# Kernel optimization log

Hardware: AMD Instinct MI355X
Metric: run time of the kernel (lower is better)

## Reference

```python
import jax, jax.numpy as jnp
import numpy as np
import math

H = 1024
N2 = 32  # N // 2 complex modes
L_LEN = 4096
LOG_DT_MIN = math.log(0.001)
LOG_DT_MAX = math.log(0.1)


def setup_inputs() -> dict:
    key = jax.random.key(0)
    k1, k2 = jax.random.split(key, 2)
    # log_dt ~ Uniform(log dt_min, log dt_max)
    log_dt = jax.random.uniform(k1, (H,), dtype=jnp.float32) * (LOG_DT_MAX - LOG_DT_MIN) + LOG_DT_MIN
    # C stored as real view of complex (H, N2): last dim = (real, imag)
    C = jax.random.normal(k2, (H, N2, 2), dtype=jnp.float32)
    log_A_real = jnp.log(0.5 * jnp.ones((H, N2), dtype=jnp.float32))
    A_imag = (math.pi * jnp.arange(N2, dtype=jnp.float32))[None, :] * jnp.ones((H, 1), jnp.float32)
    return {"log_dt": log_dt, "C": C, "log_A_real": log_A_real, "A_imag": A_imag, "L": L_LEN}


def reference(log_dt, C, log_A_real, A_imag, L):
    # dt: (H,)
    dt = jnp.exp(log_dt)
    # complex C: (H, N2)
    Cc = C[..., 0] + 1j * C[..., 1]
    # A = -exp(log_A_real) + i*A_imag : (H, N2)
    A = -jnp.exp(log_A_real) + 1j * A_imag
    dtA = A * dt[:, None]  # (H, N2)
    # discretized coefficient: C * (exp(dtA)-1)/A  (ZOH-like)
    Ck = Cc * (jnp.exp(dtA) - 1.0) / A  # (H, N2)
    # Vandermonde: exp(dtA * l) for l in [0, L)  -> (H, N2, L)
    V = jnp.exp(dtA[..., None] * jnp.arange(L, dtype=jnp.float32))
    # K = 2 * Re( sum_n Ck[h,n] * V[h,n,l] )  -> (H, L)
    K = 2.0 * jnp.einsum('hn,hnl->hl', Ck, V).real
    return K
```

## Files before the change

kernel.cpp:

```cpp
#include <hip/hip_runtime.h>
#include <math.h>


#define N2 32
#define L_LEN 4096
#define NTHREADS 256
#define JTILE (L_LEN / NTHREADS)

__global__ __launch_bounds__(NTHREADS) void s4d_gen_kernel(
    const float* __restrict__ log_dt,
    const float* __restrict__ Cri,
    const float* __restrict__ log_A_real,
    const float* __restrict__ A_imag,
    float* __restrict__ out)
{
  const int h = blockIdx.x;
  const int t = threadIdx.x;

  __shared__ double s_yrev[N2];
  __shared__ float s_x[N2], s_ckr[N2], s_cki[N2];
  __shared__ float s_Wr[N2], s_Wi[N2], s_p[N2], s_q[N2];

  if (t < N2) {
    const int n = t;
    const double dt = exp((double)log_dt[h]);
    const double Ar = -exp((double)log_A_real[h * N2 + n]);
    const double Ai = (double)A_imag[h * N2 + n];
    const double xr = dt * Ar;
    const double xi = dt * Ai;
    const double ex = exp(xr);
    const double wr = ex * cos(xi);
    const double wi = ex * sin(xi);
    const double nr = wr - 1.0, ni = wi;
    const double inv = 1.0 / (Ar * Ar + Ai * Ai);
    const double fr = (nr * Ar + ni * Ai) * inv;
    const double fi = (ni * Ar - nr * Ai) * inv;
    const double c0 = (double)Cri[(h * N2 + n) * 2 + 0];
    const double c1 = (double)Cri[(h * N2 + n) * 2 + 1];
    s_ckr[n] = (float)(2.0 * (c0 * fr - c1 * fi));
    s_cki[n] = (float)(2.0 * (c0 * fi + c1 * fr));
    s_x[n]    = (float)xr;
    s_yrev[n] = xi * 0.15915494309189535;
    double ar = wr, ai2 = wi;
#pragma unroll
    for (int k = 0; k < 8; ++k) {
      const double tr = ar * ar - ai2 * ai2;
      const double ti = 2.0 * ar * ai2;
      ar = tr; ai2 = ti;
    }
    s_Wr[n] = (float)ar;
    s_Wi[n] = (float)ai2;
    s_p[n]  = (float)(2.0 * ar);
    s_q[n]  = (float)(ar * ar + ai2 * ai2);
  }
  __syncthreads();

  float acc[JTILE];
#pragma unroll
  for (int j = 0; j < JTILE; ++j) acc[j] = 0.0f;

  const float  tf = (float)t;
  const double td = (double)t;

  for (int n = 0; n < N2; ++n) {
    double ph = s_yrev[n] * td;
    ph -= floor(ph);
    const float frac = (float)ph;
    const float sn = __builtin_amdgcn_sinf(frac);
    const float cs = __builtin_amdgcn_cosf(frac);
    const float e  = __expf(s_x[n] * tf);
    const float vr = e * cs;
    const float vi = e * sn;
    const float ckr = s_ckr[n], cki = s_cki[n];
    const float ur = fmaf(ckr, vr, -(cki * vi));
    const float ui = fmaf(ckr, vi,  cki * vr);
    float s0 = ur;
    float s1 = fmaf(ur, s_Wr[n], -(ui * s_Wi[n]));
    acc[0] += s0;
    acc[1] += s1;
    const float p = s_p[n], q = s_q[n];
#pragma unroll
    for (int j = 2; j < JTILE; ++j) {
      const float s2 = fmaf(p, s1, -(q * s0));
      acc[j] += s2;
      s0 = s1; s1 = s2;
    }
  }

  float* o = out + (size_t)h * L_LEN + t;
#pragma unroll
  for (int j = 0; j < JTILE; ++j) o[j * NTHREADS] = acc[j];
}

extern "C" void kernel_launch(void* const* d_in, const int* in_sizes, int n_in,
                              void* d_out, int out_size, void* d_ws, size_t ws_size,
                              hipStream_t stream) {
  const float* log_dt     = (const float*)d_in[0];
  const float* Cri        = (const float*)d_in[1];
  const float* log_A_real = (const float*)d_in[2];
  const float* A_imag     = (const float*)d_in[3];
  float* out = (float*)d_out;
  const int H = in_sizes[0];

  s4d_gen_kernel<<<dim3(H), dim3(NTHREADS), 0, stream>>>(
      log_dt, Cri, log_A_real, A_imag, out);
}
```

Before: 79.50 us.

## Split coefficient prep into separate kernel and split sequence length across blocks

Per-mode FP64 coefficient setup moves out of each block into a separate fully parallel prep kernel. Previously only 32 of 256 threads did this work while the rest waited at a barrier. Results go to workspace in global memory as a packed struct plus a double array. The main kernel now uses a 2D grid, with each block covering half of the sequence and each thread computing 8 outputs instead of 16. This doubles the blocks for occupancy, but also doubles the per-mode transcendental setup per output and adds a second launch and global coefficient reads.

```diff
diff --git a/kernel.cpp b/kernel.cpp
--- a/kernel.cpp
+++ b/kernel.cpp
@@ -5,89 +5,103 @@
 #define N2 32
 #define L_LEN 4096
 #define NTHREADS 256
-#define JTILE (L_LEN / NTHREADS)
+#define JTILE 8
+#define HALF_L 2048
 
-__global__ __launch_bounds__(NTHREADS) void s4d_gen_kernel(
+struct Coef {
+  float x;
+  float ckr, cki;
+  float Wr, Wi;
+  float p, q;
+  float pad;
+};
+
+__global__ __launch_bounds__(256) void s4d_prep_kernel(
     const float* __restrict__ log_dt,
     const float* __restrict__ Cri,
     const float* __restrict__ log_A_real,
     const float* __restrict__ A_imag,
+    double* __restrict__ yrev,
+    Coef* __restrict__ cf)
+{
+  const int idx = blockIdx.x * 256 + threadIdx.x;
+  const int h = idx >> 5;
+
+  const double dt = exp((double)log_dt[h]);
+  const double Ar = -exp((double)log_A_real[idx]);
+  const double Ai = (double)A_imag[idx];
+  const double xr = dt * Ar;
+  const double xi = dt * Ai;
+  const double ex = exp(xr);
+  const double wr = ex * cos(xi);
+  const double wi = ex * sin(xi);
+  const double nr = wr - 1.0, ni = wi;
+  const double inv = 1.0 / (Ar * Ar + Ai * Ai);
+  const double fr = (nr * Ar + ni * Ai) * inv;
+  const double fi = (ni * Ar - nr * Ai) * inv;
+  const double c0 = (double)Cri[idx * 2 + 0];
+  const double c1 = (double)Cri[idx * 2 + 1];
+  double ar = wr, ai = wi;
+#pragma unroll
+  for (int k = 0; k < 8; ++k) {
+    const double tr = ar * ar - ai * ai;
+    const double ti = 2.0 * ar * ai;
+    ar = tr; ai = ti;
+  }
+  Coef c;
+  c.x   = (float)xr;
+  c.ckr = (float)(2.0 * (c0 * fr - c1 * fi));
+  c.cki = (float)(2.0 * (c0 * fi + c1 * fr));
+  c.Wr  = (float)ar;
+  c.Wi  = (float)ai;
+  c.p   = (float)(2.0 * ar);
+  c.q   = (float)(ar * ar + ai * ai);
+  c.pad = 0.0f;
+  cf[idx] = c;
+  yrev[idx] = xi * 0.15915494309189535;
+}
+
+__global__ __launch_bounds__(NTHREADS) void s4d_main_kernel(
+    const double* __restrict__ yrev,
+    const Coef* __restrict__ cf,
     float* __restrict__ out)
 {
   const int h = blockIdx.x;
-  const int t = threadIdx.x;
-
-  __shared__ double s_yrev[N2];
-  __shared__ float s_x[N2], s_ckr[N2], s_cki[N2];
-  __shared__ float s_Wr[N2], s_Wi[N2], s_p[N2], s_q[N2];
-
-  if (t < N2) {
-    const int n = t;
-    const double dt = exp((double)log_dt[h]);
-    const double Ar = -exp((double)log_A_real[h * N2 + n]);
-    const double Ai = (double)A_imag[h * N2 + n];
-    const double xr = dt * Ar;
-    const double xi = dt * Ai;
-    const double ex = exp(xr);
-    const double wr = ex * cos(xi);
-    const double wi = ex * sin(xi);
-    const double nr = wr - 1.0, ni = wi;
-    const double inv = 1.0 / (Ar * Ar + Ai * Ai);
-    const double fr = (nr * Ar + ni * Ai) * inv;
-    const double fi = (ni * Ar - nr * Ai) * inv;
-    const double c0 = (double)Cri[(h * N2 + n) * 2 + 0];
-    const double c1 = (double)Cri[(h * N2 + n) * 2 + 1];
-    s_ckr[n] = (float)(2.0 * (c0 * fr - c1 * fi));
-    s_cki[n] = (float)(2.0 * (c0 * fi + c1 * fr));
-    s_x[n]    = (float)xr;
-    s_yrev[n] = xi * 0.15915494309189535;
-    double ar = wr, ai2 = wi;
-#pragma unroll
-    for (int k = 0; k < 8; ++k) {
-      const double tr = ar * ar - ai2 * ai2;
-      const double ti = 2.0 * ar * ai2;
-      ar = tr; ai2 = ti;
-    }
-    s_Wr[n] = (float)ar;
-    s_Wi[n] = (float)ai2;
-    s_p[n]  = (float)(2.0 * ar);
-    s_q[n]  = (float)(ar * ar + ai2 * ai2);
-  }
-  __syncthreads();
+  const int l0 = blockIdx.y * HALF_L + threadIdx.x;
+  const float  lf = (float)l0;
+  const double ld = (double)l0;
 
   float acc[JTILE];
 #pragma unroll
   for (int j = 0; j < JTILE; ++j) acc[j] = 0.0f;
 
-  const float  tf = (float)t;
-  const double td = (double)t;
-
+  const int base = h * N2;
+#pragma unroll 4
   for (int n = 0; n < N2; ++n) {
-    double ph = s_yrev[n] * td;
+    const Coef c = cf[base + n];
+    double ph = yrev[base + n] * ld;
     ph -= floor(ph);
     const float frac = (float)ph;
     const float sn = __builtin_amdgcn_sinf(frac);
     const float cs = __builtin_amdgcn_cosf(frac);
-    const float e  = __expf(s_x[n] * tf);
+    const float e  = __expf(c.x * lf);
     const float vr = e * cs;
     const float vi = e * sn;
-    const float ckr = s_ckr[n], cki = s_cki[n];
-    const float ur = fmaf(ckr, vr, -(cki * vi));
-    const float ui = fmaf(ckr, vi,  cki * vr);
+    const float ur = fmaf(c.ckr, vr, -(c.cki * vi));
+    const float ui = fmaf(c.ckr, vi,  c.cki * vr);
     float s0 = ur;
-    float s1 = fmaf(ur, s_Wr[n], -(ui * s_Wi[n]));
+    float s1 = fmaf(ur, c.Wr, -(ui * c.Wi));
     acc[0] += s0;
     acc[1] += s1;
-    const float p = s_p[n], q = s_q[n];
 #pragma unroll
     for (int j = 2; j < JTILE; ++j) {
-      const float s2 = fmaf(p, s1, -(q * s0));
+      const float s2 = fmaf(c.p, s1, -(c.q * s0));
       acc[j] += s2;
       s0 = s1; s1 = s2;
     }
   }
 
-  float* o = out + (size_t)h * L_LEN + t;
+  float* o = out + (size_t)h * L_LEN + l0;
 #pragma unroll
   for (int j = 0; j < JTILE; ++j) o[j * NTHREADS] = acc[j];
 }
@@ -102,6 +116,10 @@
   float* out = (float*)d_out;
   const int H = in_sizes[0];
 
-  s4d_gen_kernel<<<dim3(H), dim3(NTHREADS), 0, stream>>>(
-      log_dt, Cri, log_A_real, A_imag, out);
+  double* yrev = (double*)d_ws;
+  Coef*   cf   = (Coef*)((char*)d_ws + (size_t)H * N2 * sizeof(double));
+
+  s4d_prep_kernel<<<dim3(H * N2 / 256), dim3(256), 0, stream>>>(
+      log_dt, Cri, log_A_real, A_imag, yrev, cf);
+  s4d_main_kernel<<<dim3(H, 2), dim3(NTHREADS), 0, stream>>>(yrev, cf, out);
 }
```

Result: slower. 86.41 us (+8.7%).

## Factor Vandermonde into power tables and evaluate via per-thread dot products

Applied to the files above, without the earlier changes.

Splits the work into a prep kernel and a main kernel. The prep kernel computes per-mode power tables W^(16a), Ck·W^b and W^(256j) into the workspace. The main kernel forms W^(16a+b) products per thread and reduces over modes with dot products against the W^256 table, replacing the per-thread sin/cos/exp and the second-order recurrence. This adds a second launch, workspace traffic, and float power accumulation whose error may grow for large exponents.

```diff
diff --git a/kernel.cpp b/kernel.cpp
--- a/kernel.cpp
+++ b/kernel.cpp
@@ -5,91 +5,128 @@
 #define N2 32
 #define L_LEN 4096
 #define NTHREADS 256
-#define JTILE (L_LEN / NTHREADS)
 
-__global__ __launch_bounds__(NTHREADS) void s4d_gen_kernel(
+#define PQ_STRIDE 32
+#define A2OFF (1024 * 1024)
+
+__global__ __launch_bounds__(256) void s4d_prep_kernel(
     const float* __restrict__ log_dt,
     const float* __restrict__ Cri,
     const float* __restrict__ log_A_real,
     const float* __restrict__ A_imag,
+    float2* __restrict__ ws2)
+{
+  const int idx = blockIdx.x * 256 + threadIdx.x;
+  const int h = idx >> 5;
+  const int n = idx & 31;
+
+  const double dt = exp((double)log_dt[h]);
+  const double Ar = -exp((double)log_A_real[idx]);
+  const double Ai = (double)A_imag[idx];
+  const double xr = dt * Ar;
+  const double xi = dt * Ai;
+  const double ex = exp(xr);
+  const double wr = ex * cos(xi);
+  const double wi = ex * sin(xi);
+  const double nr = wr - 1.0, ni = wi;
+  const double inv = 1.0 / (Ar * Ar + Ai * Ai);
+  const double fr = (nr * Ar + ni * Ai) * inv;
+  const double fi = (ni * Ar - nr * Ai) * inv;
+  const double c0 = (double)Cri[idx * 2 + 0];
+  const double c1 = (double)Cri[idx * 2 + 1];
+  const float ckr = (float)(2.0 * (c0 * fr - c1 * fi));
+  const float cki = (float)(2.0 * (c0 * fi + c1 * fr));
+
+  double ar = wr, ai2 = wi;
+#pragma unroll
+  for (int k = 0; k < 4; ++k) {
+    const double tr = ar * ar - ai2 * ai2;
+    const double ti = 2.0 * ar * ai2;
+    ar = tr; ai2 = ti;
+  }
+  const float w16r = (float)ar, w16i = (float)ai2;
+#pragma unroll
+  for (int k = 0; k < 4; ++k) {
+    const double tr = ar * ar - ai2 * ai2;
+    const double ti = 2.0 * ar * ai2;
+    ar = tr; ai2 = ti;
+  }
+  const float w256r = (float)ar, w256i = (float)ai2;
+  const float wfr = (float)wr, wfi = (float)wi;
+
+  float2* pq = ws2 + (size_t)idx * PQ_STRIDE;
+  float pr = 1.0f, pi = 0.0f;
+#pragma unroll
+  for (int a = 0; a < 16; ++a) {
+    pq[a] = make_float2(pr, pi);
+    const float tr = fmaf(pr, w16r, -(pi * w16i));
+    const float ti = fmaf(pr, w16i, pi * w16r);
+    pr = tr; pi = ti;
+  }
+  float qr = ckr, qi = cki;
+#pragma unroll
+  for (int b = 0; b < 16; ++b) {
+    pq[16 + b] = make_float2(qr, qi);
+    const float tr = fmaf(qr, wfr, -(qi * wfi));
+    const float ti = fmaf(qr, wfi, qi * wfr);
+    qr = tr; qi = ti;
+  }
+  float2* a2 = ws2 + A2OFF + (size_t)h * (16 * N2) + n;
+  float sr = 1.0f, si = 0.0f;
+#pragma unroll
+  for (int j = 0; j < 16; ++j) {
+    a2[j * N2] = make_float2(sr, si);
+    const float tr = fmaf(sr, w256r, -(si * w256i));
+    const float ti = fmaf(sr, w256i, si * w256r);
+    sr = tr; si = ti;
+  }
+}
+
+__global__ __launch_bounds__(NTHREADS, 4) void s4d_main_kernel(
+    const float2* __restrict__ ws2,
     float* __restrict__ out)
 {
   const int h = blockIdx.x;
   const int t = threadIdx.x;
+  const int a = t >> 4;
+  const int b = t & 15;
 
-  __shared__ double s_yrev[N2];
-  __shared__ float s_x[N2], s_ckr[N2], s_cki[N2];
-  __shared__ float s_Wr[N2], s_Wi[N2], s_p[N2], s_q[N2];
-
-  if (t < N2) {
-    const int n = t;
-    const double dt = exp((double)log_dt[h]);
-    const double Ar = -exp((double)log_A_real[h * N2 + n]);
-    const double Ai = (double)A_imag[h * N2 + n];
-    const double xr = dt * Ar;
-    const double xi = dt * Ai;
-    const double ex = exp(xr);
-    const double wr = ex * cos(xi);
-    const double wi = ex * sin(xi);
-    const double nr = wr - 1.0, ni = wi;
-    const double inv = 1.0 / (Ar * Ar + Ai * Ai);
-    const double fr = (nr * Ar + ni * Ai) * inv;
-    const double fi = (ni * Ar - nr * Ai) * inv;
-    const double c0 = (double)Cri[(h * N2 + n) * 2 + 0];
-    const double c1 = (double)Cri[(h * N2 + n) * 2 + 1];
-    s_ckr[n] = (float)(2.0 * (c0 * fr - c1 * fi));
-    s_cki[n] = (float)(2.0 * (c0 * fi + c1 * fr));
-    s_x[n]    = (float)xr;
-    s_yrev[n] = xi * 0.15915494309189535;
-    double ar = wr, ai2 = wi;
+  __shared__ float2 sPQ[N2 * PQ_STRIDE];
+  {
+    const float4* src = (const float4*)(ws2 + (size_t)h * N2 * PQ_STRIDE);
+    float4* dst = (float4*)sPQ;
 #pragma unroll
-    for (int k = 0; k < 8; ++k) {
-      const double tr = ar * ar - ai2 * ai2;
-      const double ti = 2.0 * ar * ai2;
-      ar = tr; ai2 = ti;
-    }
-    s_Wr[n] = (float)ar;
-    s_Wi[n] = (float)ai2;
-    s_p[n]  = (float)(2.0 * ar);
-    s_q[n]  = (float)(ar * ar + ai2 * ai2);
+    for (int i = 0; i < 2; ++i) dst[t + i * NTHREADS] = src[t + i * NTHREADS];
   }
   __syncthreads();
 
-  float acc[JTILE];
+  float br[N2], bi[N2];
 #pragma unroll
-  for (int j = 0; j < JTILE; ++j) acc[j] = 0.0f;
+  for (int n = 0; n < N2; ++n) {
+    const float2 P = sPQ[n * PQ_STRIDE + a];
+    const float2 Q = sPQ[n * PQ_STRIDE + 16 + b];
+    br[n] = fmaf(P.x, Q.x, -(P.y * Q.y));
+    bi[n] = fmaf(P.x, Q.y, P.y * Q.x);
+  }
 
-  const float  tf = (float)t;
-  const double td = (double)t;
-
-  for (int n = 0; n < N2; ++n) {
-    double ph = s_yrev[n] * td;
-    ph -= floor(ph);
-    const float frac = (float)ph;
-    const float sn = __builtin_amdgcn_sinf(frac);
-    const float cs = __builtin_amdgcn_cosf(frac);
-    const float e  = __expf(s_x[n] * tf);
-    const float vr = e * cs;
-    const float vi = e * sn;
-    const float ckr = s_ckr[n], cki = s_cki[n];
-    const float ur = fmaf(ckr, vr, -(cki * vi));
-    const float ui = fmaf(ckr, vi,  cki * vr);
-    float s0 = ur;
-    float s1 = fmaf(ur, s_Wr[n], -(ui * s_Wi[n]));
-    acc[0] += s0;
-    acc[1] += s1;
-    const float p = s_p[n], q = s_q[n];
+  const float2* a2h = ws2 + A2OFF + (size_t)h * (16 * N2);
+  float acc[16];
+#pragma unroll 4
+  for (int j = 0; j < 16; ++j) {
+    const float2* row = a2h + j * N2;
+    float s = 0.0f;
 #pragma unroll
-    for (int j = 2; j < JTILE; ++j) {
-      const float s2 = fmaf(p, s1, -(q * s0));
-      acc[j] += s2;
-      s0 = s1; s1 = s2;
+    for (int n = 0; n < N2; ++n) {
+      const float2 a2 = row[n];
+      s = fmaf(a2.x, br[n], s);
+      s = fmaf(-a2.y, bi[n], s);
     }
+    acc[j] = s;
   }
 
   float* o = out + (size_t)h * L_LEN + t;
 #pragma unroll
-  for (int j = 0; j < JTILE; ++j) o[j * NTHREADS] = acc[j];
+  for (int j = 0; j < 16; ++j) o[j * NTHREADS] = acc[j];
 }
 
 extern "C" void kernel_launch(void* const* d_in, const int* in_sizes, int n_in,
@@ -102,6 +139,9 @@
   float* out = (float*)d_out;
   const int H = in_sizes[0];
 
-  s4d_gen_kernel<<<dim3(H), dim3(NTHREADS), 0, stream>>>(
-      log_dt, Cri, log_A_real, A_imag, out);
+  float2* ws2 = (float2*)d_ws;
+
+  s4d_prep_kernel<<<dim3(H * N2 / 256), dim3(256), 0, stream>>>(
+      log_dt, Cri, log_A_real, A_imag, ws2);
+  s4d_main_kernel<<<dim3(H), dim3(NTHREADS), 0, stream>>>(ws2, out);
 }
```

After: 159.0 us. 2x slower.

## Replace per-thread transcendental phase with precomputed power tables in shared memory

Applied to the files above, without the earlier changes.

Each thread's starting value w^t was previously computed with a double-precision phase reduction plus sin, cos and exp for every mode. It is now formed as a product of two table entries, P[a]=w^(16a) and Q[b]=Ck*w^b, where t=16a+b. Two warps fill these tables in shared memory, so the main loop needs only a complex multiply per mode. This removes the double-precision floor and the transcendental calls from the hot loop, at the cost of an extra barrier and shared-memory traffic. Accuracy may differ because the powers are built by repeated float multiplication. The launch bounds also add a minimum-blocks hint.

```diff
diff --git a/kernel.cpp b/kernel.cpp
--- a/kernel.cpp
+++ b/kernel.cpp
@@ -5,9 +5,8 @@
 #define N2 32
 #define L_LEN 4096
 #define NTHREADS 256
-#define JTILE (L_LEN / NTHREADS)
 
-__global__ __launch_bounds__(NTHREADS) void s4d_gen_kernel(
+__global__ __launch_bounds__(NTHREADS, 4) void s4d_fused_kernel(
     const float* __restrict__ log_dt,
     const float* __restrict__ Cri,
     const float* __restrict__ log_A_real,
@@ -16,16 +15,20 @@
 {
   const int h = blockIdx.x;
   const int t = threadIdx.x;
+  const int a = t >> 4;
+  const int b = t & 15;
 
-  __shared__ double s_yrev[N2];
-  __shared__ float s_x[N2], s_ckr[N2], s_cki[N2];
-  __shared__ float s_Wr[N2], s_Wi[N2], s_p[N2], s_q[N2];
+  __shared__ float2 s_w[N2], s_w16[N2], s_ck[N2];
+  __shared__ float4 s_Wpq[N2];
+  __shared__ float2 s_P[16 * N2];
+  __shared__ float2 s_Q[16 * N2];
 
   if (t < N2) {
     const int n = t;
+    const int idx = h * N2 + n;
     const double dt = exp((double)log_dt[h]);
-    const double Ar = -exp((double)log_A_real[h * N2 + n]);
-    const double Ai = (double)A_imag[h * N2 + n];
+    const double Ar = -exp((double)log_A_real[idx]);
+    const double Ai = (double)A_imag[idx];
     const double xr = dt * Ar;
     const double xi = dt * Ai;
     const double ex = exp(xr);
@@ -35,53 +38,78 @@
     const double inv = 1.0 / (Ar * Ar + Ai * Ai);
     const double fr = (nr * Ar + ni * Ai) * inv;
     const double fi = (ni * Ar - nr * Ai) * inv;
-    const double c0 = (double)Cri[(h * N2 + n) * 2 + 0];
-    const double c1 = (double)Cri[(h * N2 + n) * 2 + 1];
-    s_ckr[n] = (float)(2.0 * (c0 * fr - c1 * fi));
-    s_cki[n] = (float)(2.0 * (c0 * fi + c1 * fr));
-    s_x[n]    = (float)xr;
-    s_yrev[n] = xi * 0.15915494309189535;
+    const double c0 = (double)Cri[idx * 2 + 0];
+    const double c1 = (double)Cri[idx * 2 + 1];
+    s_ck[n] = make_float2((float)(2.0 * (c0 * fr - c1 * fi)),
+                          (float)(2.0 * (c0 * fi + c1 * fr)));
+    s_w[n] = make_float2((float)wr, (float)wi);
     double ar = wr, ai2 = wi;
 #pragma unroll
-    for (int k = 0; k < 8; ++k) {
+    for (int k = 0; k < 4; ++k) {
       const double tr = ar * ar - ai2 * ai2;
       const double ti = 2.0 * ar * ai2;
       ar = tr; ai2 = ti;
     }
-    s_Wr[n] = (float)ar;
-    s_Wi[n] = (float)ai2;
-    s_p[n]  = (float)(2.0 * ar);
-    s_q[n]  = (float)(ar * ar + ai2 * ai2);
+    s_w16[n] = make_float2((float)ar, (float)ai2);
+#pragma unroll
+    for (int k = 0; k < 4; ++k) {
+      const double tr = ar * ar - ai2 * ai2;
+      const double ti = 2.0 * ar * ai2;
+      ar = tr; ai2 = ti;
+    }
+    s_Wpq[n] = make_float4((float)ar, (float)ai2,
+                           (float)(2.0 * ar), (float)(ar * ar + ai2 * ai2));
   }
   __syncthreads();
 
-  float acc[JTILE];
+  if (t < 64) {
+    const int n = t & 31;
+    if (t < 32) {
+      const float2 g = s_w16[n];
+      float pr = 1.0f, pi = 0.0f;
 #pragma unroll
-  for (int j = 0; j < JTILE; ++j) acc[j] = 0.0f;
+      for (int aa = 0; aa < 16; ++aa) {
+        s_P[aa * N2 + n] = make_float2(pr, pi);
+        const float tr = fmaf(pr, g.x, -(pi * g.y));
+        const float ti = fmaf(pr, g.y, pi * g.x);
+        pr = tr; pi = ti;
+      }
+    } else {
+      const float2 w = s_w[n];
+      const float2 c = s_ck[n];
+      float qr = c.x, qi = c.y;
+#pragma unroll
+      for (int bb = 0; bb < 16; ++bb) {
+        s_Q[bb * N2 + n] = make_float2(qr, qi);
+        const float tr = fmaf(qr, w.x, -(qi * w.y));
+        const float ti = fmaf(qr, w.y, qi * w.x);
+        qr = tr; qi = ti;
+      }
+    }
+  }
+  __syncthreads();
 
-  const float  tf = (float)t;
-  const double td = (double)t;
+  float acc[16];
+#pragma unroll
+  for (int j = 0; j < 16; ++j) acc[j] = 0.0f;
 
+  const float2* Pa = s_P + a * N2;
+  const float2* Qb = s_Q + b * N2;
+
+#pragma unroll 2
   for (int n = 0; n < N2; ++n) {
-    double ph = s_yrev[n] * td;
-    ph -= floor(ph);
-    const float frac = (float)ph;
-    const float sn = __builtin_amdgcn_sinf(frac);
-    const float cs = __builtin_amdgcn_cosf(frac);
-    const float e  = __expf(s_x[n] * tf);
-    const float vr = e * cs;
-    const float vi = e * sn;
-    const float ckr = s_ckr[n], cki = s_cki[n];
-    const float ur = fmaf(ckr, vr, -(cki * vi));
-    const float ui = fmaf(ckr, vi,  cki * vr);
-    float s0 = ur;
-    float s1 = fmaf(ur, s_Wr[n], -(ui * s_Wi[n]));
+    const float2 P = Pa[n];
+    const float2 Q = Qb[n];
+    const float4 W = s_Wpq[n];
+    const float Br = fmaf(P.x, Q.x, -(P.y * Q.y));
+    const float Bi = fmaf(P.x, Q.y, P.y * Q.x);
+    float s0 = Br;
+    float s1 = fmaf(Br, W.x, -(Bi * W.y));
     acc[0] += s0;
     acc[1] += s1;
-    const float p = s_p[n], q = s_q[n];
 #pragma unroll
-    for (int j = 2; j < JTILE; ++j) {
-      const float s2 = fmaf(p, s1, -(q * s0));
+    for (int j = 2; j < 16; ++j) {
+      const float s2 = fmaf(W.z, s1, -(W.w * s0));
       acc[j] += s2;
       s0 = s1; s1 = s2;
     }
@@ -89,7 +117,7 @@
 
   float* o = out + (size_t)h * L_LEN + t;
 #pragma unroll
-  for (int j = 0; j < JTILE; ++j) o[j * NTHREADS] = acc[j];
+  for (int j = 0; j < 16; ++j) o[j * NTHREADS] = acc[j];
 }
 
 extern "C" void kernel_launch(void* const* d_in, const int* in_sizes, int n_in,
@@ -102,6 +130,6 @@
   float* out = (float*)d_out;
   const int H = in_sizes[0];
 
-  s4d_gen_kernel<<<dim3(H), dim3(NTHREADS), 0, stream>>>(
+  s4d_fused_kernel<<<dim3(H), dim3(NTHREADS), 0, stream>>>(
       log_dt, Cri, log_A_real, A_imag, out);
 }
```

Measured after the change: 77.95 us. Within noise of the previous version (-2.0%).
